# Kernel tuning notes

Measured on AMD Instinct MI355X. Metric: run time of the kernel, lower is better.

The kernel has to match this reference:

```python
import jax, jax.numpy as jnp
import numpy as np

B, T, D_IN, D_LAT, N_UNITS = 2048, 200, 64, 64, 100


def setup_inputs() -> dict:
    key = jax.random.key(0)
    ks = jax.random.split(key, 20)
    s = 0.05
    inp = {
        "data": jax.random.normal(ks[0], (B, T, D_IN), dtype=jnp.float32),
        "time_steps": jnp.arange(T, dtype=jnp.float32),
        # ODE func: 2-layer MLP latent -> n_units -> latent (tanh hidden)
        "Wf1": jax.random.normal(ks[1], (D_LAT, N_UNITS), jnp.float32) * s,
        "bf1": jnp.zeros((N_UNITS,), jnp.float32),
        "Wf2": jax.random.normal(ks[2], (N_UNITS, D_LAT), jnp.float32) * s,
        "bf2": jnp.zeros((D_LAT,), jnp.float32),
        # GRU update gate net: [latent+input] -> n_units -> latent
        "Wz1": jax.random.normal(ks[3], (D_LAT + D_IN, N_UNITS), jnp.float32) * s,
        "bz1": jnp.zeros((N_UNITS,), jnp.float32),
        "Wz2": jax.random.normal(ks[4], (N_UNITS, D_LAT), jnp.float32) * s,
        "bz2": jnp.zeros((D_LAT,), jnp.float32),
        # GRU reset gate net
        "Wr1": jax.random.normal(ks[5], (D_LAT + D_IN, N_UNITS), jnp.float32) * s,
        "br1": jnp.zeros((N_UNITS,), jnp.float32),
        "Wr2": jax.random.normal(ks[6], (N_UNITS, D_LAT), jnp.float32) * s,
        "br2": jnp.zeros((D_LAT,), jnp.float32),
        # GRU candidate-state net
        "Wh1": jax.random.normal(ks[7], (D_LAT + D_IN, N_UNITS), jnp.float32) * s,
        "bh1": jnp.zeros((N_UNITS,), jnp.float32),
        "Wh2": jax.random.normal(ks[8], (N_UNITS, D_LAT), jnp.float32) * s,
        "bh2": jnp.zeros((D_LAT,), jnp.float32),
    }
    return inp


def _mlp(x, W1, b1, W2, b2):
    return jnp.tanh(x @ W1 + b1) @ W2 + b2


def reference(data, time_steps, Wf1, bf1, Wf2, bf2,
              Wz1, bz1, Wz2, bz2, Wr1, br1, Wr2, br2,
              Wh1, bh1, Wh2, bh2):
    n_traj = data.shape[0]
    latent_dim = Wf1.shape[0]
    prev_y0 = jnp.zeros((n_traj, latent_dim), dtype=data.dtype)

    # Faithful to original control flow: with uniform arange time steps,
    # |prev_t - t_i| < minimum_step always holds -> single explicit Euler step.
    # Original code swaps (prev_t, t_i) at the end of each iteration, so the
    # effective dt at iteration i is: i==1 -> ts[1]-ts[0]; i>=2 -> ts[i-2]-ts[i-1].
    dts = jnp.concatenate([time_steps[1:2] - time_steps[0:1],
                           time_steps[:-2] - time_steps[1:-1]])  # [T-1]

    xs_data = jnp.moveaxis(data[:, 1:, :], 0, 1)  # [T-1, B, D_in]

    def step(prev_y, inp):
        x, dt = inp
        # Euler step of the neural ODE
        yi_ode = prev_y + _mlp(prev_y, Wf1, bf1, Wf2, bf2) * dt
        # GRU update (GRUUnitOriginal): gates from concat(y_ode, x)
        c = jnp.concatenate([yi_ode, x], axis=-1)
        z = jax.nn.sigmoid(_mlp(c, Wz1, bz1, Wz2, bz2))
        r = jax.nn.sigmoid(_mlp(c, Wr1, br1, Wr2, br2))
        ch = jnp.concatenate([yi_ode * r, x], axis=-1)
        h = jnp.tanh(_mlp(ch, Wh1, bh1, Wh2, bh2))
        y = (1.0 - z) * h + z * yi_ode
        return y, y

    yi, ys = jax.lax.scan(step, prev_y0, (xs_data, dts))
    latent_ys = jnp.moveaxis(ys, 0, 1)  # [B, T-1, latent]
    return yi, latent_ys
```

## Files before the change

kernel.cpp:

```cpp
#include <hip/hip_runtime.h>


#define NBT   2048
#define TSTEP 200
#define NT    8

typedef short s8v __attribute__((ext_vector_type(8)));
typedef float f4v __attribute__((ext_vector_type(4)));

#define RB_Y 144
#define RB_C 272
#define OFF_Y  0
#define OFF_C  2304
#define OFF_HF 6656
#define OFF_HZ 11008
#define OFF_HR 15360
#define OFF_HH 19712
#define SMEM_TOT 24064

__device__ __forceinline__ unsigned cvtpk(float lo, float hi) {
    unsigned r;
    asm("v_cvt_pk_bf16_f32 %0, %1, %2" : "=v"(r) : "v"(lo), "v"(hi));
    return r;
}
__device__ __forceinline__ unsigned short f2bf(float f) {
    unsigned int b = __float_as_uint(f);
    return (unsigned short)((b + 0x7fffu + ((b >> 16) & 1u)) >> 16);
}
__device__ __forceinline__ float bf2f(unsigned short u) {
    return __uint_as_float(((unsigned)u) << 16);
}
__device__ __forceinline__ float tanh_f(float x) {
    float e = __expf(2.0f * x);
    return fmaf(-2.0f, __builtin_amdgcn_rcpf(e + 1.0f), 1.0f);
}
__device__ __forceinline__ float sigm_f(float x) {
    return __builtin_amdgcn_rcpf(1.0f + __expf(-x));
}
__device__ __forceinline__ f4v mfma16(s8v a, s8v b, f4v c) {
    return __builtin_amdgcn_mfma_f32_16x16x32_bf16(a, b, c, 0, 0, 0);
}
__device__ __forceinline__ f4v splat(float b) { f4v v = {b, b, b, b}; return v; }

__device__ __forceinline__ s8v load_bfrag(const float* __restrict__ W,
                                          int Ncols, int Krows, int k0, int n) {
    s8v r;
#pragma unroll
    for (int j = 0; j < 8; ++j) {
        const int k = k0 + j;
        const float v = (k < Krows && n < Ncols) ? W[k * Ncols + n] : 0.0f;
        r[j] = (short)f2bf(v);
    }
    return r;
}

template <int RB>
__device__ __forceinline__ s8v load_af(const char* base, int lane, int kt) {
    return *(const s8v*)(base + (lane & 15) * RB + ((lane >> 4) * 16) + kt * 64);
}

__device__ __forceinline__ void store4(char* base, int col2, int rb, int pitch,
                                       float v0, float v1, float v2, float v3) {
    const unsigned u01 = cvtpk(v0, v1), u23 = cvtpk(v2, v3);
    *(short*)(base + (rb + 0) * pitch + col2) = (short)(u01 & 0xffffu);
    *(short*)(base + (rb + 1) * pitch + col2) = (short)(u01 >> 16);
    *(short*)(base + (rb + 2) * pitch + col2) = (short)(u23 & 0xffffu);
    *(short*)(base + (rb + 3) * pitch + col2) = (short)(u23 >> 16);
}
__device__ __forceinline__ void store_tanh(char* base, int n0, int lane, f4v a) {
    store4(base, (n0 + (lane & 15)) * 2, (lane >> 4) * 4, RB_C,
           tanh_f(a[0]), tanh_f(a[1]), tanh_f(a[2]), tanh_f(a[3]));
}

__global__ __launch_bounds__(512, 2) void ode_rnn_mfma8(
    const float* __restrict__ data, const float* __restrict__ tsv,
    const float* __restrict__ Wf1, const float* __restrict__ bf1,
    const float* __restrict__ Wf2, const float* __restrict__ bf2,
    const float* __restrict__ Wz1, const float* __restrict__ bz1,
    const float* __restrict__ Wz2, const float* __restrict__ bz2,
    const float* __restrict__ Wr1, const float* __restrict__ br1,
    const float* __restrict__ Wr2, const float* __restrict__ br2,
    const float* __restrict__ Wh1, const float* __restrict__ bh1,
    const float* __restrict__ Wh2, const float* __restrict__ bh2,
    float* __restrict__ out_yi, float* __restrict__ out_ys)
{
    __shared__ __align__(16) char smem[SMEM_TOT];

    const int tid  = threadIdx.x;
    const int lane = tid & 63;
    const int wv   = tid >> 6;
    const bool isA = (wv < 4);
    const int b0   = blockIdx.x * NT;

    for (int i = tid; i < SMEM_TOT / 4; i += 512) ((unsigned*)smem)[i] = 0u;

    const int kb = (lane >> 4) * 8;
    const int n1 = wv * 16 + (lane & 15);
    const int n2 = (wv & 3) * 16 + (lane & 15);

    s8v Bf1[2], Bz1[4], Br1[4], Bh1[4];
    s8v Bf2[4], Bz2[4], Bh2[4], Br2[4];
#pragma unroll
    for (int kt = 0; kt < 2; ++kt)
        Bf1[kt] = load_bfrag(Wf1, 100, 64, kt * 32 + kb, n1);
#pragma unroll
    for (int kt = 0; kt < 4; ++kt) {
        Bz1[kt] = load_bfrag(Wz1, 100, 128, kt * 32 + kb, n1);
        Br1[kt] = load_bfrag(Wr1, 100, 128, kt * 32 + kb, n1);
        Bh1[kt] = load_bfrag(Wh1, 100, 128, kt * 32 + kb, n1);
    }
    if (isA) {
#pragma unroll
        for (int kt = 0; kt < 4; ++kt) {
            Bf2[kt] = load_bfrag(Wf2, 64, 100, kt * 32 + kb, n2);
            Bz2[kt] = load_bfrag(Wz2, 64, 100, kt * 32 + kb, n2);
            Bh2[kt] = load_bfrag(Wh2, 64, 100, kt * 32 + kb, n2);
        }
    } else {
#pragma unroll
        for (int kt = 0; kt < 4; ++kt)
            Br2[kt] = load_bfrag(Wr2, 64, 100, kt * 32 + kb, n2);
    }

    const float b1f = (n1 < 100) ? bf1[n1] : 0.0f;
    const float b1z = (n1 < 100) ? bz1[n1] : 0.0f;
    const float b1r = (n1 < 100) ? br1[n1] : 0.0f;
    const float b1h = (n1 < 100) ? bh1[n1] : 0.0f;
    const float bF2 = isA ? bf2[n2] : 0.0f;
    const float bZ2 = isA ? bz2[n2] : 0.0f;
    const float bH2 = isA ? bh2[n2] : 0.0f;
    const float bR2 = isA ? 0.0f : br2[n2];

    const int t2  = tid & 255;
    const int xtr = t2 >> 5;
    const int xd  = (t2 & 31) * 2;

    const int col2 = n2 * 2;
    const int rb   = (lane >> 4) * 4;

    f4v y_reg = splat(0.0f), yode = splat(0.0f), zf = splat(0.0f);
    __syncthreads();

    for (int s = 0; s < TSTEP - 1; ++s) {
        float2 xv;
        if (!isA)
            xv = *(const float2*)&data[((size_t)(b0 + xtr) * TSTEP + (s + 1)) * 64 + xd];
        const float dt = (s == 0) ? (tsv[1] - tsv[0]) : (tsv[s - 1] - tsv[s]);

        {
            const s8v ya0 = load_af<RB_Y>(smem + OFF_Y, lane, 0);
            const s8v ya1 = load_af<RB_Y>(smem + OFF_Y, lane, 1);
            f4v a = splat(b1f);
            a = mfma16(ya0, Bf1[0], a);
            a = mfma16(ya1, Bf1[1], a);
            store_tanh(smem + OFF_HF, wv * 16, lane, a);
        }
        __syncthreads();

        if (isA) {
            f4v ac = splat(bF2);
#pragma unroll
            for (int kt = 0; kt < 4; ++kt)
                ac = mfma16(load_af<RB_C>(smem + OFF_HF, lane, kt), Bf2[kt], ac);
#pragma unroll
            for (int r = 0; r < 4; ++r) yode[r] = fmaf(dt, ac[r], y_reg[r]);
            store4(smem + OFF_C, col2, rb, RB_C, yode[0], yode[1], yode[2], yode[3]);
        } else {
            *(unsigned*)(smem + OFF_C + xtr * RB_C + 128 + (t2 & 31) * 4) =
                cvtpk(xv.x, xv.y);
        }
        __syncthreads();

        {
            const s8v c0 = load_af<RB_C>(smem + OFF_C, lane, 0);
            const s8v c1 = load_af<RB_C>(smem + OFF_C, lane, 1);
            const s8v c2 = load_af<RB_C>(smem + OFF_C, lane, 2);
            const s8v c3 = load_af<RB_C>(smem + OFF_C, lane, 3);
            f4v az = splat(b1z), ar = splat(b1r);
            az = mfma16(c0, Bz1[0], az); az = mfma16(c1, Bz1[1], az);
            az = mfma16(c2, Bz1[2], az); az = mfma16(c3, Bz1[3], az);
            ar = mfma16(c0, Br1[0], ar); ar = mfma16(c1, Br1[1], ar);
            ar = mfma16(c2, Br1[2], ar); ar = mfma16(c3, Br1[3], ar);
            store_tanh(smem + OFF_HZ, wv * 16, lane, az);
            store_tanh(smem + OFF_HR, wv * 16, lane, ar);
        }
        __syncthreads();

        if (isA) {
            f4v az = splat(bZ2);
#pragma unroll
            for (int kt = 0; kt < 4; ++kt)
                az = mfma16(load_af<RB_C>(smem + OFF_HZ, lane, kt), Bz2[kt], az);
#pragma unroll
            for (int r = 0; r < 4; ++r) zf[r] = sigm_f(az[r]);
        } else {
            f4v ar = splat(bR2);
#pragma unroll
            for (int kt = 0; kt < 4; ++kt)
                ar = mfma16(load_af<RB_C>(smem + OFF_HR, lane, kt), Br2[kt], ar);
            float ch[4];
#pragma unroll
            for (int r = 0; r < 4; ++r) {
                const unsigned short yv =
                    *(const unsigned short*)(smem + OFF_C + (rb + r) * RB_C + col2);
                ch[r] = bf2f(yv) * sigm_f(ar[r]);
            }
            store4(smem + OFF_C, col2, rb, RB_C, ch[0], ch[1], ch[2], ch[3]);
        }
        __syncthreads();

        {
            const s8v d0 = load_af<RB_C>(smem + OFF_C, lane, 0);
            const s8v d1 = load_af<RB_C>(smem + OFF_C, lane, 1);
            const s8v d2 = load_af<RB_C>(smem + OFF_C, lane, 2);
            const s8v d3 = load_af<RB_C>(smem + OFF_C, lane, 3);
            f4v ah = splat(b1h);
            ah = mfma16(d0, Bh1[0], ah); ah = mfma16(d1, Bh1[1], ah);
            ah = mfma16(d2, Bh1[2], ah); ah = mfma16(d3, Bh1[3], ah);
            store_tanh(smem + OFF_HH, wv * 16, lane, ah);
        }
        __syncthreads();

        if (isA) {
            f4v ah = splat(bH2);
#pragma unroll
            for (int kt = 0; kt < 4; ++kt)
                ah = mfma16(load_af<RB_C>(smem + OFF_HH, lane, kt), Bh2[kt], ah);
#pragma unroll
            for (int r = 0; r < 4; ++r) {
                const float h = tanh_f(ah[r]);
                y_reg[r] = (1.0f - zf[r]) * h + zf[r] * yode[r];
            }
            store4(smem + OFF_Y, col2, rb, RB_Y, y_reg[0], y_reg[1], y_reg[2], y_reg[3]);
            if (lane < 32) {
#pragma unroll
                for (int r = 0; r < 4; ++r) {
                    const int row = rb + r;
                    out_ys[((size_t)(b0 + row) * (TSTEP - 1) + s) * 64 + n2] = y_reg[r];
                }
                if (s == TSTEP - 2) {
#pragma unroll
                    for (int r = 0; r < 4; ++r)
                        out_yi[(size_t)(b0 + rb + r) * 64 + n2] = y_reg[r];
                }
            }
        }
        __syncthreads();
    }
}

extern "C" void kernel_launch(void* const* d_in, const int* in_sizes, int n_in,
                              void* d_out, int out_size, void* d_ws, size_t ws_size,
                              hipStream_t stream) {
    const float* data = (const float*)d_in[0];
    const float* tsv  = (const float*)d_in[1];
    const float* Wf1 = (const float*)d_in[2];  const float* bf1 = (const float*)d_in[3];
    const float* Wf2 = (const float*)d_in[4];  const float* bf2 = (const float*)d_in[5];
    const float* Wz1 = (const float*)d_in[6];  const float* bz1 = (const float*)d_in[7];
    const float* Wz2 = (const float*)d_in[8];  const float* bz2 = (const float*)d_in[9];
    const float* Wr1 = (const float*)d_in[10]; const float* br1 = (const float*)d_in[11];
    const float* Wr2 = (const float*)d_in[12]; const float* br2 = (const float*)d_in[13];
    const float* Wh1 = (const float*)d_in[14]; const float* bh1 = (const float*)d_in[15];
    const float* Wh2 = (const float*)d_in[16]; const float* bh2 = (const float*)d_in[17];

    float* out_yi = (float*)d_out;
    float* out_ys = out_yi + (size_t)NBT * 64;

    ode_rnn_mfma8<<<NBT / NT, 512, 0, stream>>>(
        data, tsv, Wf1, bf1, Wf2, bf2, Wz1, bz1, Wz2, bz2,
        Wr1, br1, Wr2, br2, Wh1, bh1, Wh2, bh2, out_yi, out_ys);
}
```

Baseline: 355.5 us.

## Split gate work across 16 waves and stage second-layer weights in LDS

The block grows from 8 to 16 waves with three roles. Four extra waves handle the reset-gate first layer, so each wave issues fewer MFMAs per step on the serial recurrence. The second-layer weights now live transposed as bf16 in dynamic shared memory instead of registers, to cut register pressure. The next step's input is prefetched one iteration early. The trade-off is more LDS traffic on each step, a larger LDS footprint, and a launch bound that may force tight register limits or spills.

```diff
diff --git a/kernel.cpp b/kernel.cpp
--- a/kernel.cpp
+++ b/kernel.cpp
@@ -10,13 +10,18 @@
 
 #define RB_Y 144
 #define RB_C 272
-#define OFF_Y  0
-#define OFF_C  2304
-#define OFF_HF 6656
-#define OFF_HZ 11008
-#define OFF_HR 15360
-#define OFF_HH 19712
-#define SMEM_TOT 24064
+#define RB_W 272
+#define OFF_Y   0
+#define OFF_C   2304
+#define OFF_HF  6656
+#define OFF_HZ  11008
+#define OFF_HR  15360
+#define OFF_HH  19712
+#define OFF_WF2 24064
+#define OFF_WZ2 41472
+#define OFF_WR2 58880
+#define OFF_WH2 76288
+#define SMEM_TOT 93696
 
 __device__ __forceinline__ unsigned cvtpk(float lo, float hi) {
     unsigned r;
@@ -48,8 +53,8 @@
 #pragma unroll
     for (int j = 0; j < 8; ++j) {
         const int k = k0 + j;
-        const float v = (k < Krows && n < Ncols) ? W[k * Ncols + n] : 0.0f;
-        r[j] = (short)f2bf(v);
+        const float v = (k < Krows && n < Ncols) ? W[k * Ncols + j == j ? n : n] : 0.0f;
+        r[j] = (short)f2bf((k < Krows && n < Ncols) ? W[k * Ncols + n] : 0.0f);
     }
     return r;
 }
@@ -72,7 +77,15 @@
            tanh_f(a[0]), tanh_f(a[1]), tanh_f(a[2]), tanh_f(a[3]));
 }
 
-__global__ __launch_bounds__(512, 2) void ode_rnn_mfma8(
+__device__ void stage_w2t(const float* __restrict__ W, char* __restrict__ dst,
+                          int tid) {
+    for (int idx = tid; idx < 6400; idx += 1024) {
+        const int k = idx >> 6, n = idx & 63;
+        *(unsigned short*)(dst + n * RB_W + k * 2) = f2bf(W[idx]);
+    }
+}
+
+__global__ __launch_bounds__(1024, 4) void ode_rnn_16w(
     const float* __restrict__ data, const float* __restrict__ tsv,
     const float* __restrict__ Wf1, const float* __restrict__ bf1,
     const float* __restrict__ Wf2, const float* __restrict__ bf2,
@@ -84,90 +97,91 @@
     const float* __restrict__ Wh2, const float* __restrict__ bh2,
     float* __restrict__ out_yi, float* __restrict__ out_ys)
 {
-    __shared__ __align__(16) char smem[SMEM_TOT];
+    extern __shared__ __align__(16) char smem[];
 
     const int tid  = threadIdx.x;
     const int lane = tid & 63;
     const int wv   = tid >> 6;
-    const bool isA = (wv < 4);
+    const int role = (wv < 4) ? 0 : (wv < 8) ? 1 : 2;
     const int b0   = blockIdx.x * NT;
 
-    for (int i = tid; i < SMEM_TOT / 4; i += 512) ((unsigned*)smem)[i] = 0u;
-
-    const int kb = (lane >> 4) * 8;
-    const int n1 = wv * 16 + (lane & 15);
-    const int n2 = (wv & 3) * 16 + (lane & 15);
-
-    s8v Bf1[2], Bz1[4], Br1[4], Bh1[4];
-    s8v Bf2[4], Bz2[4], Bh2[4], Br2[4];
-#pragma unroll
-    for (int kt = 0; kt < 2; ++kt)
-        Bf1[kt] = load_bfrag(Wf1, 100, 64, kt * 32 + kb, n1);
-#pragma unroll
-    for (int kt = 0; kt < 4; ++kt) {
-        Bz1[kt] = load_bfrag(Wz1, 100, 128, kt * 32 + kb, n1);
-        Br1[kt] = load_bfrag(Wr1, 100, 128, kt * 32 + kb, n1);
-        Bh1[kt] = load_bfrag(Wh1, 100, 128, kt * 32 + kb, n1);
-    }
-    if (isA) {
+    for (int i = tid; i < SMEM_TOT / 4; i += 1024) ((unsigned*)smem)[i] = 0u;
+    __syncthreads();
+    stage_w2t(Wf2, smem + OFF_WF2, tid);
+    stage_w2t(Wz2, smem + OFF_WZ2, tid);
+    stage_w2t(Wr2, smem + OFF_WR2, tid);
+    stage_w2t(Wh2, smem + OFF_WH2, tid);
+
+    const int kb  = (lane >> 4) * 8;
+    const int wt1 = (role == 2) ? (wv - 8) : wv;
+    const int n1  = wt1 * 16 + (lane & 15);
+    s8v B1[10];
+    float b1a = 0.0f, b1z = 0.0f, b1h = 0.0f;
+    if (role == 2) {
+#pragma unroll
+        for (int kt = 0; kt < 4; ++kt)
+            B1[kt] = load_bfrag(Wr1, 100, 128, kt * 32 + kb, n1);
+        b1a = (n1 < 100) ? br1[n1] : 0.0f;
+    } else {
+        B1[0] = load_bfrag(Wf1, 100, 64, 0 * 32 + kb, n1);
+        B1[1] = load_bfrag(Wf1, 100, 64, 1 * 32 + kb, n1);
 #pragma unroll
         for (int kt = 0; kt < 4; ++kt) {
-            Bf2[kt] = load_bfrag(Wf2, 64, 100, kt * 32 + kb, n2);
-            Bz2[kt] = load_bfrag(Wz2, 64, 100, kt * 32 + kb, n2);
-            Bh2[kt] = load_bfrag(Wh2, 64, 100, kt * 32 + kb, n2);
-        }
-    } else {
-#pragma unroll
-        for (int kt = 0; kt < 4; ++kt)
-            Br2[kt] = load_bfrag(Wr2, 64, 100, kt * 32 + kb, n2);
-    }
-
-    const float b1f = (n1 < 100) ? bf1[n1] : 0.0f;
-    const float b1z = (n1 < 100) ? bz1[n1] : 0.0f;
-    const float b1r = (n1 < 100) ? br1[n1] : 0.0f;
-    const float b1h = (n1 < 100) ? bh1[n1] : 0.0f;
-    const float bF2 = isA ? bf2[n2] : 0.0f;
-    const float bZ2 = isA ? bz2[n2] : 0.0f;
-    const float bH2 = isA ? bh2[n2] : 0.0f;
-    const float bR2 = isA ? 0.0f : br2[n2];
+            B1[2 + kt] = load_bfrag(Wz1, 100, 128, kt * 32 + kb, n1);
+            B1[6 + kt] = load_bfrag(Wh1, 100, 128, kt * 32 + kb, n1);
+        }
+        b1a = (n1 < 100) ? bf1[n1] : 0.0f;
+        b1z = (n1 < 100) ? bz1[n1] : 0.0f;
+        b1h = (n1 < 100) ? bh1[n1] : 0.0f;
+    }
+
+    const int tw2  = wv & 3;
+    const int n2   = tw2 * 16 + (lane & 15);
+    const int col2 = n2 * 2;
+    const int rb   = (lane >> 4) * 4;
+    const float bF2 = (role == 0) ? bf2[n2] : 0.0f;
+    const float bZ2 = (role == 0) ? bz2[n2] : 0.0f;
+    const float bH2 = (role == 0) ? bh2[n2] : 0.0f;
+    const bool  xw  = (wv >= 8 && wv < 12);
+    const float bR2 = xw ? br2[n2] : 0.0f;
 
     const int t2  = tid & 255;
     const int xtr = t2 >> 5;
     const int xd  = (t2 & 31) * 2;
-
-    const int col2 = n2 * 2;
-    const int rb   = (lane >> 4) * 4;
+    float2 xv = {0.0f, 0.0f};
+    if (xw)
+        xv = *(const float2*)&data[((size_t)(b0 + xtr) * TSTEP + 1) * 64 + xd];
 
     f4v y_reg = splat(0.0f), yode = splat(0.0f), zf = splat(0.0f);
     __syncthreads();
 
     for (int s = 0; s < TSTEP - 1; ++s) {
-        float2 xv;
-        if (!isA)
-            xv = *(const float2*)&data[((size_t)(b0 + xtr) * TSTEP + (s + 1)) * 64 + xd];
         const float dt = (s == 0) ? (tsv[1] - tsv[0]) : (tsv[s - 1] - tsv[s]);
 
-        {
+        if (role < 2) {
             const s8v ya0 = load_af<RB_Y>(smem + OFF_Y, lane, 0);
             const s8v ya1 = load_af<RB_Y>(smem + OFF_Y, lane, 1);
-            f4v a = splat(b1f);
-            a = mfma16(ya0, Bf1[0], a);
-            a = mfma16(ya1, Bf1[1], a);
-            store_tanh(smem + OFF_HF, wv * 16, lane, a);
-        }
-        __syncthreads();
-
-        if (isA) {
+            f4v a = splat(b1a);
+            a = mfma16(ya0, B1[0], a);
+            a = mfma16(ya1, B1[1], a);
+            store_tanh(smem + OFF_HF, wt1 * 16, lane, a);
+        } else if (xw) {
+            *(unsigned*)(smem + OFF_C + xtr * RB_C + 128 + (t2 & 31) * 4) =
+                cvtpk(xv.x, xv.y);
+            const int snx = (s + 2 < TSTEP) ? (s + 2) : (TSTEP - 1);
+            xv = *(const float2*)&data[((size_t)(b0 + xtr) * TSTEP + snx) * 64 + xd];
+        }
+        __syncthreads();
+
+        if (role == 0) {
             f4v ac = splat(bF2);
 #pragma unroll
             for (int kt = 0; kt < 4; ++kt)
-                ac = mfma16(load_af<RB_C>(smem + OFF_HF, lane, kt), Bf2[kt], ac);
+                ac = mfma16(load_af<RB_C>(smem + OFF_HF, lane, kt),
+                            load_af<RB_W>(smem + OFF_WF2 + tw2 * 16 * RB_W, lane, kt), ac);
 #pragma unroll
             for (int r = 0; r < 4; ++r) yode[r] = fmaf(dt, ac[r], y_reg[r]);
             store4(smem + OFF_C, col2, rb, RB_C, yode[0], yode[1], yode[2], yode[3]);
-        } else {
-            *(unsigned*)(smem + OFF_C + xtr * RB_C + 128 + (t2 & 31) * 4) =
-                cvtpk(xv.x, xv.y);
         }
         __syncthreads();
 
@@ -176,28 +190,34 @@
             const s8v c1 = load_af<RB_C>(smem + OFF_C, lane, 1);
             const s8v c2 = load_af<RB_C>(smem + OFF_C, lane, 2);
             const s8v c3 = load_af<RB_C>(smem + OFF_C, lane, 3);
-            f4v az = splat(b1z), ar = splat(b1r);
-            az = mfma16(c0, Bz1[0], az); az = mfma16(c1, Bz1[1], az);
-            az = mfma16(c2, Bz1[2], az); az = mfma16(c3, Bz1[3], az);
-            ar = mfma16(c0, Br1[0], ar); ar = mfma16(c1, Br1[1], ar);
-            ar = mfma16(c2, Br1[2], ar); ar = mfma16(c3, Br1[3], ar);
-            store_tanh(smem + OFF_HZ, wv * 16, lane, az);
-            store_tanh(smem + OFF_HR, wv * 16, lane, ar);
-        }
-        __syncthreads();
-
-        if (isA) {
+            if (role == 2) {
+                f4v ar = splat(b1a);
+                ar = mfma16(c0, B1[0], ar); ar = mfma16(c1, B1[1], ar);
+                ar = mfma16(c2, B1[2], ar); ar = mfma16(c3, B1[3], ar);
+                store_tanh(smem + OFF_HR, wt1 * 16, lane, ar);
+            } else {
+                f4v az = splat(b1z);
+                az = mfma16(c0, B1[2], az); az = mfma16(c1, B1[3], az);
+                az = mfma16(c2, B1[4], az); az = mfma16(c3, B1[5], az);
+                store_tanh(smem + OFF_HZ, wt1 * 16, lane, az);
+            }
+        }
+        __syncthreads();
+
+        if (role == 0) {
             f4v az = splat(bZ2);
 #pragma unroll
             for (int kt = 0; kt < 4; ++kt)
-                az = mfma16(load_af<RB_C>(smem + OFF_HZ, lane, kt), Bz2[kt], az);
+                az = mfma16(load_af<RB_C>(smem + OFF_HZ, lane, kt),
+                            load_af<RB_W>(smem + OFF_WZ2 + tw2 * 16 * RB_W, lane, kt), az);
 #pragma unroll
             for (int r = 0; r < 4; ++r) zf[r] = sigm_f(az[r]);
-        } else {
+        } else if (xw) {
             f4v ar = splat(bR2);
 #pragma unroll
             for (int kt = 0; kt < 4; ++kt)
-                ar = mfma16(load_af<RB_C>(smem + OFF_HR, lane, kt), Br2[kt], ar);
+                ar = mfma16(load_af<RB_C>(smem + OFF_HR, lane, kt),
+                            load_af<RB_W>(smem + OFF_WR2 + tw2 * 16 * RB_W, lane, kt), ar);
             float ch[4];
 #pragma unroll
             for (int r = 0; r < 4; ++r) {
@@ -209,23 +229,24 @@
         }
         __syncthreads();
 
-        {
+        if (role < 2) {
             const s8v d0 = load_af<RB_C>(smem + OFF_C, lane, 0);
             const s8v d1 = load_af<RB_C>(smem + OFF_C, lane, 1);
             const s8v d2 = load_af<RB_C>(smem + OFF_C, lane, 2);
             const s8v d3 = load_af<RB_C>(smem + OFF_C, lane, 3);
             f4v ah = splat(b1h);
-            ah = mfma16(d0, Bh1[0], ah); ah = mfma16(d1, Bh1[1], ah);
-            ah = mfma16(d2, Bh1[2], ah); ah = mfma16(d3, Bh1[3], ah);
-            store_tanh(smem + OFF_HH, wv * 16, lane, ah);
-        }
-        __syncthreads();
-
-        if (isA) {
+            ah = mfma16(d0, B1[6], ah); ah = mfma16(d1, B1[7], ah);
+            ah = mfma16(d2, B1[8], ah); ah = mfma16(d3, B1[9], ah);
+            store_tanh(smem + OFF_HH, wt1 * 16, lane, ah);
+        }
+        __syncthreads();
+
+        if (role == 0) {
             f4v ah = splat(bH2);
 #pragma unroll
             for (int kt = 0; kt < 4; ++kt)
-                ah = mfma16(load_af<RB_C>(smem + OFF_HH, lane, kt), Bh2[kt], ah);
+                ah = mfma16(load_af<RB_C>(smem + OFF_HH, lane, kt),
+                            load_af<RB_W>(smem + OFF_WH2 + tw2 * 16 * RB_W, lane, kt), ah);
 #pragma unroll
             for (int r = 0; r < 4; ++r) {
                 const float h = tanh_f(ah[r]);
@@ -234,10 +255,9 @@
             store4(smem + OFF_Y, col2, rb, RB_Y, y_reg[0], y_reg[1], y_reg[2], y_reg[3]);
             if (lane < 32) {
 #pragma unroll
-                for (int r = 0; r < 4; ++r) {
-                    const int row = rb + r;
-                    out_ys[((size_t)(b0 + row) * (TSTEP - 1) + s) * 64 + n2] = y_reg[r];
-                }
+                for (int r = 0; r < 4; ++r)
+                    out_ys[((size_t)(b0 + rb + r) * (TSTEP - 1) + s) * 64 + n2] =
+                        y_reg[r];
                 if (s == TSTEP - 2) {
 #pragma unroll
                     for (int r = 0; r < 4; ++r)
@@ -266,7 +286,10 @@
     float* out_yi = (float*)d_out;
     float* out_ys = out_yi + (size_t)NBT * 64;
 
-    ode_rnn_mfma8<<<NBT / NT, 512, 0, stream>>>(
+    (void)hipFuncSetAttribute((const void*)ode_rnn_16w,
+                              hipFuncAttributeMaxDynamicSharedMemorySize, SMEM_TOT);
+
+    ode_rnn_16w<<<NBT / NT, 1024, SMEM_TOT, stream>>>(
         data, tsv, Wf1, bf1, Wf2, bf2, Wz1, bz1, Wz2, bz2,
         Wr1, br1, Wr2, br2, Wh1, bh1, Wh2, bh2, out_yi, out_ys);
 }
```

After: 426.1 us. 19.9% more time.

## Split MFMA accumulation chains, add setprio, defer global stores, mask padding-row stores

Applied to the files above, without the earlier changes.

Each 4-deep dependent MFMA accumulation chain is split into two independent 2-deep chains that are summed afterwards, which shortens the latency-bound critical path of every recurrent step. MFMA sections are wrapped in s_setprio to favour the issuing wave. The out_ys global store for a step is moved to the start of the next step, so it sits off the tail before the barrier, and the last step is written after the loop. LDS stores are restricted to lanes < 32, since only 8 of the 16 tile rows are real trajectories, which removes redundant tanh work and LDS writes.

```diff
diff --git a/kernel.cpp b/kernel.cpp
--- a/kernel.cpp
+++ b/kernel.cpp
@@ -68,11 +68,12 @@
     *(short*)(base + (rb + 3) * pitch + col2) = (short)(u23 >> 16);
 }
 __device__ __forceinline__ void store_tanh(char* base, int n0, int lane, f4v a) {
-    store4(base, (n0 + (lane & 15)) * 2, (lane >> 4) * 4, RB_C,
-           tanh_f(a[0]), tanh_f(a[1]), tanh_f(a[2]), tanh_f(a[3]));
-}
-
-__global__ __launch_bounds__(512, 2) void ode_rnn_mfma8(
+    if (lane < 32)
+        store4(base, (n0 + (lane & 15)) * 2, (lane >> 4) * 4, RB_C,
+               tanh_f(a[0]), tanh_f(a[1]), tanh_f(a[2]), tanh_f(a[3]));
+}
+
+__global__ __launch_bounds__(512, 2) void ode_rnn_r9(
     const float* __restrict__ data, const float* __restrict__ tsv,
     const float* __restrict__ Wf1, const float* __restrict__ bf1,
     const float* __restrict__ Wf2, const float* __restrict__ bf2,
@@ -147,24 +148,40 @@
             xv = *(const float2*)&data[((size_t)(b0 + xtr) * TSTEP + (s + 1)) * 64 + xd];
         const float dt = (s == 0) ? (tsv[1] - tsv[0]) : (tsv[s - 1] - tsv[s]);
 
+        if (isA && s > 0 && lane < 32) {
+#pragma unroll
+            for (int r = 0; r < 4; ++r)
+                out_ys[((size_t)(b0 + rb + r) * (TSTEP - 1) + (s - 1)) * 64 + n2] =
+                    y_reg[r];
+        }
+
         {
             const s8v ya0 = load_af<RB_Y>(smem + OFF_Y, lane, 0);
             const s8v ya1 = load_af<RB_Y>(smem + OFF_Y, lane, 1);
+            __builtin_amdgcn_s_setprio(1);
             f4v a = splat(b1f);
             a = mfma16(ya0, Bf1[0], a);
             a = mfma16(ya1, Bf1[1], a);
+            __builtin_amdgcn_s_setprio(0);
             store_tanh(smem + OFF_HF, wv * 16, lane, a);
         }
         __syncthreads();
 
         if (isA) {
-            f4v ac = splat(bF2);
-#pragma unroll
-            for (int kt = 0; kt < 4; ++kt)
-                ac = mfma16(load_af<RB_C>(smem + OFF_HF, lane, kt), Bf2[kt], ac);
-#pragma unroll
-            for (int r = 0; r < 4; ++r) yode[r] = fmaf(dt, ac[r], y_reg[r]);
-            store4(smem + OFF_C, col2, rb, RB_C, yode[0], yode[1], yode[2], yode[3]);
+            const s8v a0 = load_af<RB_C>(smem + OFF_HF, lane, 0);
+            const s8v a1 = load_af<RB_C>(smem + OFF_HF, lane, 1);
+            const s8v a2 = load_af<RB_C>(smem + OFF_HF, lane, 2);
+            const s8v a3 = load_af<RB_C>(smem + OFF_HF, lane, 3);
+            __builtin_amdgcn_s_setprio(1);
+            f4v acA = mfma16(a1, Bf2[1], mfma16(a0, Bf2[0], splat(bF2)));
+            f4v acB = mfma16(a3, Bf2[3], mfma16(a2, Bf2[2], splat(0.0f)));
+            __builtin_amdgcn_s_setprio(0);
+#pragma unroll
+            for (int r = 0; r < 4; ++r)
+                yode[r] = fmaf(dt, acA[r] + acB[r], y_reg[r]);
+            if (lane < 32)
+                store4(smem + OFF_C, col2, rb, RB_C,
+                       yode[0], yode[1], yode[2], yode[3]);
         } else {
             *(unsigned*)(smem + OFF_C + xtr * RB_C + 128 + (t2 & 31) * 4) =
                 cvtpk(xv.x, xv.y);
@@ -176,36 +193,47 @@
             const s8v c1 = load_af<RB_C>(smem + OFF_C, lane, 1);
             const s8v c2 = load_af<RB_C>(smem + OFF_C, lane, 2);
             const s8v c3 = load_af<RB_C>(smem + OFF_C, lane, 3);
-            f4v az = splat(b1z), ar = splat(b1r);
-            az = mfma16(c0, Bz1[0], az); az = mfma16(c1, Bz1[1], az);
-            az = mfma16(c2, Bz1[2], az); az = mfma16(c3, Bz1[3], az);
-            ar = mfma16(c0, Br1[0], ar); ar = mfma16(c1, Br1[1], ar);
-            ar = mfma16(c2, Br1[2], ar); ar = mfma16(c3, Br1[3], ar);
-            store_tanh(smem + OFF_HZ, wv * 16, lane, az);
-            store_tanh(smem + OFF_HR, wv * 16, lane, ar);
+            __builtin_amdgcn_s_setprio(1);
+            f4v azA = mfma16(c1, Bz1[1], mfma16(c0, Bz1[0], splat(b1z)));
+            f4v azB = mfma16(c3, Bz1[3], mfma16(c2, Bz1[2], splat(0.0f)));
+            f4v arA = mfma16(c1, Br1[1], mfma16(c0, Br1[0], splat(b1r)));
+            f4v arB = mfma16(c3, Br1[3], mfma16(c2, Br1[2], splat(0.0f)));
+            __builtin_amdgcn_s_setprio(0);
+            store_tanh(smem + OFF_HZ, wv * 16, lane, azA + azB);
+            store_tanh(smem + OFF_HR, wv * 16, lane, arA + arB);
         }
         __syncthreads();
 
         if (isA) {
-            f4v az = splat(bZ2);
-#pragma unroll
-            for (int kt = 0; kt < 4; ++kt)
-                az = mfma16(load_af<RB_C>(smem + OFF_HZ, lane, kt), Bz2[kt], az);
-#pragma unroll
-            for (int r = 0; r < 4; ++r) zf[r] = sigm_f(az[r]);
+            const s8v a0 = load_af<RB_C>(smem + OFF_HZ, lane, 0);
+            const s8v a1 = load_af<RB_C>(smem + OFF_HZ, lane, 1);
+            const s8v a2 = load_af<RB_C>(smem + OFF_HZ, lane, 2);
+            const s8v a3 = load_af<RB_C>(smem + OFF_HZ, lane, 3);
+            __builtin_amdgcn_s_setprio(1);
+            f4v azA = mfma16(a1, Bz2[1], mfma16(a0, Bz2[0], splat(bZ2)));
+            f4v azB = mfma16(a3, Bz2[3], mfma16(a2, Bz2[2], splat(0.0f)));
+            __builtin_amdgcn_s_setprio(0);
+#pragma unroll
+            for (int r = 0; r < 4; ++r) zf[r] = sigm_f(azA[r] + azB[r]);
         } else {
-            f4v ar = splat(bR2);
-#pragma unroll
-            for (int kt = 0; kt < 4; ++kt)
-                ar = mfma16(load_af<RB_C>(smem + OFF_HR, lane, kt), Br2[kt], ar);
-            float ch[4];
-#pragma unroll
-            for (int r = 0; r < 4; ++r) {
-                const unsigned short yv =
-                    *(const unsigned short*)(smem + OFF_C + (rb + r) * RB_C + col2);
-                ch[r] = bf2f(yv) * sigm_f(ar[r]);
+            const s8v a0 = load_af<RB_C>(smem + OFF_HR, lane, 0);
+            const s8v a1 = load_af<RB_C>(smem + OFF_HR, lane, 1);
+            const s8v a2 = load_af<RB_C>(smem + OFF_HR, lane, 2);
+            const s8v a3 = load_af<RB_C>(smem + OFF_HR, lane, 3);
+            __builtin_amdgcn_s_setprio(1);
+            f4v arA = mfma16(a1, Br2[1], mfma16(a0, Br2[0], splat(bR2)));
+            f4v arB = mfma16(a3, Br2[3], mfma16(a2, Br2[2], splat(0.0f)));
+            __builtin_amdgcn_s_setprio(0);
+            if (lane < 32) {
+                float ch[4];
+#pragma unroll
+                for (int r = 0; r < 4; ++r) {
+                    const unsigned short yv = *(const unsigned short*)
+                        (smem + OFF_C + (rb + r) * RB_C + col2);
+                    ch[r] = bf2f(yv) * sigm_f(arA[r] + arB[r]);
+                }
+                store4(smem + OFF_C, col2, rb, RB_C, ch[0], ch[1], ch[2], ch[3]);
             }
-            store4(smem + OFF_C, col2, rb, RB_C, ch[0], ch[1], ch[2], ch[3]);
         }
         __syncthreads();
 
@@ -214,38 +242,42 @@
             const s8v d1 = load_af<RB_C>(smem + OFF_C, lane, 1);
             const s8v d2 = load_af<RB_C>(smem + OFF_C, lane, 2);
             const s8v d3 = load_af<RB_C>(smem + OFF_C, lane, 3);
-            f4v ah = splat(b1h);
-            ah = mfma16(d0, Bh1[0], ah); ah = mfma16(d1, Bh1[1], ah);
-            ah = mfma16(d2, Bh1[2], ah); ah = mfma16(d3, Bh1[3], ah);
-            store_tanh(smem + OFF_HH, wv * 16, lane, ah);
+            __builtin_amdgcn_s_setprio(1);
+            f4v ahA = mfma16(d1, Bh1[1], mfma16(d0, Bh1[0], splat(b1h)));
+            f4v ahB = mfma16(d3, Bh1[3], mfma16(d2, Bh1[2], splat(0.0f)));
+            __builtin_amdgcn_s_setprio(0);
+            store_tanh(smem + OFF_HH, wv * 16, lane, ahA + ahB);
         }
         __syncthreads();
 
         if (isA) {
-            f4v ah = splat(bH2);
-#pragma unroll
-            for (int kt = 0; kt < 4; ++kt)
-                ah = mfma16(load_af<RB_C>(smem + OFF_HH, lane, kt), Bh2[kt], ah);
+            const s8v a0 = load_af<RB_C>(smem + OFF_HH, lane, 0);
+            const s8v a1 = load_af<RB_C>(smem + OFF_HH, lane, 1);
+            const s8v a2 = load_af<RB_C>(smem + OFF_HH, lane, 2);
+            const s8v a3 = load_af<RB_C>(smem + OFF_HH, lane, 3);
+            __builtin_amdgcn_s_setprio(1);
+            f4v ahA = mfma16(a1, Bh2[1], mfma16(a0, Bh2[0], splat(bH2)));
+            f4v ahB = mfma16(a3, Bh2[3], mfma16(a2, Bh2[2], splat(0.0f)));
+            __builtin_amdgcn_s_setprio(0);
 #pragma unroll
             for (int r = 0; r < 4; ++r) {
-                const float h = tanh_f(ah[r]);
+                const float h = tanh_f(ahA[r] + ahB[r]);
                 y_reg[r] = (1.0f - zf[r]) * h + zf[r] * yode[r];
             }
-            store4(smem + OFF_Y, col2, rb, RB_Y, y_reg[0], y_reg[1], y_reg[2], y_reg[3]);
-            if (lane < 32) {
-#pragma unroll
-                for (int r = 0; r < 4; ++r) {
-                    const int row = rb + r;
-                    out_ys[((size_t)(b0 + row) * (TSTEP - 1) + s) * 64 + n2] = y_reg[r];
-                }
-                if (s == TSTEP - 2) {
-#pragma unroll
-                    for (int r = 0; r < 4; ++r)
-                        out_yi[(size_t)(b0 + rb + r) * 64 + n2] = y_reg[r];
-                }
-            }
-        }
-        __syncthreads();
+            if (lane < 32)
+                store4(smem + OFF_Y, col2, rb, RB_Y,
+                       y_reg[0], y_reg[1], y_reg[2], y_reg[3]);
+        }
+        __syncthreads();
+    }
+
+    if (isA && lane < 32) {
+#pragma unroll
+        for (int r = 0; r < 4; ++r) {
+            out_ys[((size_t)(b0 + rb + r) * (TSTEP - 1) + (TSTEP - 2)) * 64 + n2] =
+                y_reg[r];
+            out_yi[(size_t)(b0 + rb + r) * 64 + n2] = y_reg[r];
+        }
     }
 }
 
@@ -266,7 +298,7 @@
     float* out_yi = (float*)d_out;
     float* out_ys = out_yi + (size_t)NBT * 64;
 
-    ode_rnn_mfma8<<<NBT / NT, 512, 0, stream>>>(
+    ode_rnn_r9<<<NBT / NT, 512, 0, stream>>>(
         data, tsv, Wf1, bf1, Wf2, bf2, Wz1, bz1, Wz2, bz2,
         Wr1, br1, Wr2, br2, Wh1, bh1, Wh2, bh2, out_yi, out_ys);
 }
```

Measured after the change: 375.6 us. +5.7%, slower.

## Precompute input projections of GRU gates one step ahead, off the critical path

Applied to the files above, without the earlier changes.

Splits each GRU first-layer matmul into latent and input halves. The input-side products (x@W for z, r and h gates, plus bias) for the next step are computed at the end of the current step from a separate x buffer that is loaded one step ahead. The per-step gate matmuls then cover only the 64 latent columns, which shortens the dependent chain between barriers. The cost is extra registers for the three precomputed accumulators and a slightly larger shared-memory footprint.

```diff
diff --git a/kernel.cpp b/kernel.cpp
--- a/kernel.cpp
+++ b/kernel.cpp
@@ -8,15 +8,16 @@
 typedef short s8v __attribute__((ext_vector_type(8)));
 typedef float f4v __attribute__((ext_vector_type(4)));
 
-#define RB_Y 144
-#define RB_C 272
+#define RB64  144
+#define RB128 272
 #define OFF_Y  0
 #define OFF_C  2304
-#define OFF_HF 6656
-#define OFF_HZ 11008
-#define OFF_HR 15360
-#define OFF_HH 19712
-#define SMEM_TOT 24064
+#define OFF_X  4608
+#define OFF_HF 6912
+#define OFF_HZ 11264
+#define OFF_HR 15616
+#define OFF_HH 19968
+#define SMEM_TOT 24320
 
 __device__ __forceinline__ unsigned cvtpk(float lo, float hi) {
     unsigned r;
@@ -68,11 +69,11 @@
     *(short*)(base + (rb + 3) * pitch + col2) = (short)(u23 >> 16);
 }
 __device__ __forceinline__ void store_tanh(char* base, int n0, int lane, f4v a) {
-    store4(base, (n0 + (lane & 15)) * 2, (lane >> 4) * 4, RB_C,
+    store4(base, (n0 + (lane & 15)) * 2, (lane >> 4) * 4, RB128,
            tanh_f(a[0]), tanh_f(a[1]), tanh_f(a[2]), tanh_f(a[3]));
 }
 
-__global__ __launch_bounds__(512, 2) void ode_rnn_mfma8(
+__global__ __launch_bounds__(512, 2) void ode_rnn_xp(
     const float* __restrict__ data, const float* __restrict__ tsv,
     const float* __restrict__ Wf1, const float* __restrict__ bf1,
     const float* __restrict__ Wf2, const float* __restrict__ bf2,
@@ -139,17 +140,35 @@
     const int rb   = (lane >> 4) * 4;
 
     f4v y_reg = splat(0.0f), yode = splat(0.0f), zf = splat(0.0f);
+
     __syncthreads();
+    if (!isA) {
+        const float2 x1 = *(const float2*)
+            &data[((size_t)(b0 + xtr) * TSTEP + 1) * 64 + xd];
+        *(unsigned*)(smem + OFF_X + xtr * RB64 + (t2 & 31) * 4) = cvtpk(x1.x, x1.y);
+    }
+    __syncthreads();
+
+    f4v xpz, xpr, xph;
+    {
+        const s8v x0 = load_af<RB64>(smem + OFF_X, lane, 0);
+        const s8v x1 = load_af<RB64>(smem + OFF_X, lane, 1);
+        xpz = mfma16(x1, Bz1[3], mfma16(x0, Bz1[2], splat(b1z)));
+        xpr = mfma16(x1, Br1[3], mfma16(x0, Br1[2], splat(b1r)));
+        xph = mfma16(x1, Bh1[3], mfma16(x0, Bh1[2], splat(b1h)));
+    }
 
     for (int s = 0; s < TSTEP - 1; ++s) {
         float2 xv;
-        if (!isA)
-            xv = *(const float2*)&data[((size_t)(b0 + xtr) * TSTEP + (s + 1)) * 64 + xd];
+        if (!isA) {
+            const int sx = (s + 2 < TSTEP) ? (s + 2) : (TSTEP - 1);
+            xv = *(const float2*)&data[((size_t)(b0 + xtr) * TSTEP + sx) * 64 + xd];
+        }
         const float dt = (s == 0) ? (tsv[1] - tsv[0]) : (tsv[s - 1] - tsv[s]);
 
         {
-            const s8v ya0 = load_af<RB_Y>(smem + OFF_Y, lane, 0);
-            const s8v ya1 = load_af<RB_Y>(smem + OFF_Y, lane, 1);
+            const s8v ya0 = load_af<RB64>(smem + OFF_Y, lane, 0);
+            const s8v ya1 = load_af<RB64>(smem + OFF_Y, lane, 1);
             f4v a = splat(b1f);
             a = mfma16(ya0, Bf1[0], a);
             a = mfma16(ya1, Bf1[1], a);
@@ -161,26 +180,21 @@
             f4v ac = splat(bF2);
 #pragma unroll
             for (int kt = 0; kt < 4; ++kt)
-                ac = mfma16(load_af<RB_C>(smem + OFF_HF, lane, kt), Bf2[kt], ac);
+                ac = mfma16(load_af<RB128>(smem + OFF_HF, lane, kt), Bf2[kt], ac);
 #pragma unroll
             for (int r = 0; r < 4; ++r) yode[r] = fmaf(dt, ac[r], y_reg[r]);
-            store4(smem + OFF_C, col2, rb, RB_C, yode[0], yode[1], yode[2], yode[3]);
+            store4(smem + OFF_C, col2, rb, RB64, yode[0], yode[1], yode[2], yode[3]);
         } else {
-            *(unsigned*)(smem + OFF_C + xtr * RB_C + 128 + (t2 & 31) * 4) =
+            *(unsigned*)(smem + OFF_X + xtr * RB64 + (t2 & 31) * 4) =
                 cvtpk(xv.x, xv.y);
         }
         __syncthreads();
 
         {
-            const s8v c0 = load_af<RB_C>(smem + OFF_C, lane, 0);
-            const s8v c1 = load_af<RB_C>(smem + OFF_C, lane, 1);
-            const s8v c2 = load_af<RB_C>(smem + OFF_C, lane, 2);
-            const s8v c3 = load_af<RB_C>(smem + OFF_C, lane, 3);
-            f4v az = splat(b1z), ar = splat(b1r);
-            az = mfma16(c0, Bz1[0], az); az = mfma16(c1, Bz1[1], az);
-            az = mfma16(c2, Bz1[2], az); az = mfma16(c3, Bz1[3], az);
-            ar = mfma16(c0, Br1[0], ar); ar = mfma16(c1, Br1[1], ar);
-            ar = mfma16(c2, Br1[2], ar); ar = mfma16(c3, Br1[3], ar);
+            const s8v c0 = load_af<RB64>(smem + OFF_C, lane, 0);
+            const s8v c1 = load_af<RB64>(smem + OFF_C, lane, 1);
+            f4v az = mfma16(c1, Bz1[1], mfma16(c0, Bz1[0], xpz));
+            f4v ar = mfma16(c1, Br1[1], mfma16(c0, Br1[0], xpr));
             store_tanh(smem + OFF_HZ, wv * 16, lane, az);
             store_tanh(smem + OFF_HR, wv * 16, lane, ar);
         }
@@ -190,33 +204,29 @@
             f4v az = splat(bZ2);
 #pragma unroll
             for (int kt = 0; kt < 4; ++kt)
-                az = mfma16(load_af<RB_C>(smem + OFF_HZ, lane, kt), Bz2[kt], az);
+                az = mfma16(load_af<RB128>(smem + OFF_HZ, lane, kt), Bz2[kt], az);
 #pragma unroll
             for (int r = 0; r < 4; ++r) zf[r] = sigm_f(az[r]);
         } else {
             f4v ar = splat(bR2);
 #pragma unroll
             for (int kt = 0; kt < 4; ++kt)
-                ar = mfma16(load_af<RB_C>(smem + OFF_HR, lane, kt), Br2[kt], ar);
+                ar = mfma16(load_af<RB128>(smem + OFF_HR, lane, kt), Br2[kt], ar);
             float ch[4];
 #pragma unroll
             for (int r = 0; r < 4; ++r) {
                 const unsigned short yv =
-                    *(const unsigned short*)(smem + OFF_C + (rb + r) * RB_C + col2);
+                    *(const unsigned short*)(smem + OFF_C + (rb + r) * RB64 + col2);
                 ch[r] = bf2f(yv) * sigm_f(ar[r]);
             }
-            store4(smem + OFF_C, col2, rb, RB_C, ch[0], ch[1], ch[2], ch[3]);
-        }
-        __syncthreads();
-
-        {
-            const s8v d0 = load_af<RB_C>(smem + OFF_C, lane, 0);
-            const s8v d1 = load_af<RB_C>(smem + OFF_C, lane, 1);
-            const s8v d2 = load_af<RB_C>(smem + OFF_C, lane, 2);
-            const s8v d3 = load_af<RB_C>(smem + OFF_C, lane, 3);
-            f4v ah = splat(b1h);
-            ah = mfma16(d0, Bh1[0], ah); ah = mfma16(d1, Bh1[1], ah);
-            ah = mfma16(d2, Bh1[2], ah); ah = mfma16(d3, Bh1[3], ah);
+            store4(smem + OFF_C, col2, rb, RB64, ch[0], ch[1], ch[2], ch[3]);
+        }
+        __syncthreads();
+
+        {
+            const s8v d0 = load_af<RB64>(smem + OFF_C, lane, 0);
+            const s8v d1 = load_af<RB64>(smem + OFF_C, lane, 1);
+            f4v ah = mfma16(d1, Bh1[1], mfma16(d0, Bh1[0], xph));
             store_tanh(smem + OFF_HH, wv * 16, lane, ah);
         }
         __syncthreads();
@@ -225,25 +235,31 @@
             f4v ah = splat(bH2);
 #pragma unroll
             for (int kt = 0; kt < 4; ++kt)
-                ah = mfma16(load_af<RB_C>(smem + OFF_HH, lane, kt), Bh2[kt], ah);
+                ah = mfma16(load_af<RB128>(smem + OFF_HH, lane, kt), Bh2[kt], ah);
 #pragma unroll
             for (int r = 0; r < 4; ++r) {
                 const float h = tanh_f(ah[r]);
                 y_reg[r] = (1.0f - zf[r]) * h + zf[r] * yode[r];
             }
-            store4(smem + OFF_Y, col2, rb, RB_Y, y_reg[0], y_reg[1], y_reg[2], y_reg[3]);
+            store4(smem + OFF_Y, col2, rb, RB64, y_reg[0], y_reg[1], y_reg[2], y_reg[3]);
             if (lane < 32) {
 #pragma unroll
-                for (int r = 0; r < 4; ++r) {
-                    const int row = rb + r;
-                    out_ys[((size_t)(b0 + row) * (TSTEP - 1) + s) * 64 + n2] = y_reg[r];
-                }
+                for (int r = 0; r < 4; ++r)
+                    out_ys[((size_t)(b0 + rb + r) * (TSTEP - 1) + s) * 64 + n2] =
+                        y_reg[r];
                 if (s == TSTEP - 2) {
 #pragma unroll
                     for (int r = 0; r < 4; ++r)
                         out_yi[(size_t)(b0 + rb + r) * 64 + n2] = y_reg[r];
                 }
             }
+        }
+        {
+            const s8v x0 = load_af<RB64>(smem + OFF_X, lane, 0);
+            const s8v x1 = load_af<RB64>(smem + OFF_X, lane, 1);
+            xpz = mfma16(x1, Bz1[3], mfma16(x0, Bz1[2], splat(b1z)));
+            xpr = mfma16(x1, Br1[3], mfma16(x0, Br1[2], splat(b1r)));
+            xph = mfma16(x1, Bh1[3], mfma16(x0, Bh1[2], splat(b1h)));
         }
         __syncthreads();
     }
@@ -266,7 +282,7 @@
     float* out_yi = (float*)d_out;
     float* out_ys = out_yi + (size_t)NBT * 64;
 
-    ode_rnn_mfma8<<<NBT / NT, 512, 0, stream>>>(
+    ode_rnn_xp<<<NBT / NT, 512, 0, stream>>>(
         data, tsv, Wf1, bf1, Wf2, bf2, Wz1, bz1, Wz2, bz2,
         Wr1, br1, Wr2, br2, Wh1, bh1, Wh2, bh2, out_yi, out_ys);
 }
```

Result: no change. 353.5 us (-0.5%).
